# Performance work log

Measured on AMD Instinct MI355X. Metric: run time of the kernel, lower is better.

The kernel has to match this reference:

```python
import jax, jax.numpy as jnp
import numpy as np


def _bag_mean(idx, table):
    # F.embedding_bag(mode='mean', padding_idx=last row): padding entries are
    # excluded from both the sum and the count. idx: [B, S, K]
    pad = table.shape[0] - 1
    mask = (idx != pad)[..., None].astype(table.dtype)          # [B,S,K,1]
    emb = table[idx] * mask                                      # [B,S,K,D]
    cnt = mask.sum(axis=-2)                                      # [B,S,1]
    s = emb.sum(axis=-2)                                         # [B,S,D]
    return jnp.where(cnt > 0, s / jnp.maximum(cnt, 1.0), 0.0)


def _subgraph_parts(qq, ques_table, skill_table, diff_table, area_table,
                    ques2skill, ques2diff, ques2area):
    qe = ques_table[qq]                                          # [B,S,D]
    sk = _bag_mean(ques2skill[qq], skill_table)                  # [B,S,D]
    df = diff_table[ques2diff[qq][..., 0]]                       # [B,S,D]
    ar = area_table[ques2area[qq][..., 0]]                       # [B,S,D]
    return qe, sk, df, ar


def reference(q, a, next_q, ques_table, skill_table, diff_table, area_table,
              ques2skill, ques2diff, ques2area, Wq, bq):
    # ---- get_subgraph_embedding (non-JunYi path) ----
    qe, sk, df, ar = _subgraph_parts(q, ques_table, skill_table, diff_table,
                                     area_table, ques2skill, ques2diff, ques2area)
    q_emb = (qe + sk + df + ar) / 4.0

    nqe, nsk, ndf, nar = _subgraph_parts(next_q, ques_table, skill_table,
                                         diff_table, area_table, ques2skill,
                                         ques2diff, ques2area)
    nq_emb = (nqe + nsk + ndf + nar) / 4.0
    # faithful to source: the averaging line for next_q is applied twice
    nq_emb = (nq_emb + nsk + ndf + nar) / 4.0

    q_emb = q_emb @ Wq.T + bq
    nq_emb = nq_emb @ Wq.T + bq

    # ---- Fusion_Module: answer==1 keeps first half, answer==0 keeps second ----
    af = a[..., None].astype(q_emb.dtype)                        # [B,S,1]
    input_emb = jnp.concatenate([q_emb * af, q_emb * (1.0 - af)], axis=-1)

    return jnp.concatenate([input_emb, nq_emb], axis=-1)        # [B,S,3D]


def setup_inputs() -> dict:
    key = jax.random.key(0)
    ks = jax.random.split(key, 12)
    B, S, D = 16, 2048, 128
    NQ, NS, ND, NA, K = 200001, 2001, 100, 50, 8
    return {
        "q": jax.random.randint(ks[0], (B, S), 0, NQ - 1),
        "a": jax.random.randint(ks[1], (B, S), 0, 2),
        "next_q": jax.random.randint(ks[2], (B, S), 0, NQ - 1),
        "ques_table": jax.random.normal(ks[3], (NQ, D), jnp.float32),
        "skill_table": jax.random.normal(ks[4], (NS, D), jnp.float32),
        "diff_table": jax.random.normal(ks[5], (ND, D), jnp.float32),
        "area_table": jax.random.normal(ks[6], (NA, D), jnp.float32),
        "ques2skill": jax.random.randint(ks[7], (NQ, K), 0, NS),
        "ques2diff": jax.random.randint(ks[8], (NQ, 1), 0, ND),
        "ques2area": jax.random.randint(ks[9], (NQ, 1), 0, NA),
        "Wq": jax.random.normal(ks[10], (D, D), jnp.float32) / np.sqrt(D),
        "bq": jax.random.normal(ks[11], (D,), jnp.float32) * 0.01,
    }
```

## Files before the change

### kernel.cpp

```cpp
#include <hip/hip_runtime.h>
#include <hip/hip_bf16.h>

typedef float  f32x4  __attribute__((ext_vector_type(4)));
typedef short  s16x8  __attribute__((ext_vector_type(8)));

#define PIN_LOADS() asm volatile("" ::: "memory")

__device__ __forceinline__ unsigned short f2bf(float f) {
    unsigned int u = __float_as_uint(f);
    unsigned int rnd = 0x7fffu + ((u >> 16) & 1u);
    return (unsigned short)((u + rnd) >> 16);
}

__device__ __forceinline__ void bf8_fma(const s16x8 v, float s, f32x4& a0, f32x4& a1) {
    const uint4 u = *(const uint4*)&v;
    a0[0] += s * __uint_as_float(u.x << 16);
    a0[1] += s * __uint_as_float(u.x & 0xffff0000u);
    a0[2] += s * __uint_as_float(u.y << 16);
    a0[3] += s * __uint_as_float(u.y & 0xffff0000u);
    a1[0] += s * __uint_as_float(u.z << 16);
    a1[1] += s * __uint_as_float(u.z & 0xffff0000u);
    a1[2] += s * __uint_as_float(u.w << 16);
    a1[3] += s * __uint_as_float(u.w & 0xffff0000u);
}

__global__ __launch_bounds__(256)
void h2kt_prep(const float* __restrict__ Wq,
               const float* __restrict__ skill, const float* __restrict__ diff,
               const float* __restrict__ area,
               const int* __restrict__ q, const int* __restrict__ next_q,
               const int* __restrict__ a_arr,
               const int* __restrict__ q2s, const int* __restrict__ q2d,
               const int* __restrict__ q2a,
               unsigned short* __restrict__ Wqb,
               unsigned short* __restrict__ T2,
               int* __restrict__ desc,
               int pad_idx)
{
    const int bid = blockIdx.x, tid = threadIdx.x;

    if (bid < 8) {
        const int s  = bid * 256 + tid;
        const int f  = s >> 6, sl = s & 63;
        const int jt = f >> 2, kt = f & 3;
        const int row = jt * 16 + (sl & 15);
        const int col = kt * 32 + (sl >> 4) * 8;
        const float4 w0 = *(const float4*)(Wq + row * 128 + col);
        const float4 w1 = *(const float4*)(Wq + row * 128 + col + 4);
        s16x8 v;
        v[0] = (short)f2bf(w0.x); v[1] = (short)f2bf(w0.y);
        v[2] = (short)f2bf(w0.z); v[3] = (short)f2bf(w0.w);
        v[4] = (short)f2bf(w1.x); v[5] = (short)f2bf(w1.y);
        v[6] = (short)f2bf(w1.z); v[7] = (short)f2bf(w1.w);
        *(s16x8*)(Wqb + (size_t)s * 8) = v;
    } else if (bid < 42) {
        const int lane = tid & 63;
        const int cl = lane & 15, grp = lane >> 4;
        const int row16 = ((bid - 8) * 4 + (tid >> 6)) * 16;
        if (row16 > 2150) return;

        int srow = row16 + cl;
        if (srow > 2150) srow = 2150;
        const float* src = (srow < 2001) ? skill + (size_t)srow * 128
                         : (srow < 2101) ? diff + (size_t)(srow - 2001) * 128
                                         : area + (size_t)(srow - 2101) * 128;
        s16x8 afr[4];
        #pragma unroll
        for (int kt = 0; kt < 4; ++kt) {
            const float4 v0 = *(const float4*)(src + kt * 32 + grp * 8);
            const float4 v1 = *(const float4*)(src + kt * 32 + grp * 8 + 4);
            s16x8 v;
            v[0] = (short)f2bf(v0.x); v[1] = (short)f2bf(v0.y);
            v[2] = (short)f2bf(v0.z); v[3] = (short)f2bf(v0.w);
            v[4] = (short)f2bf(v1.x); v[5] = (short)f2bf(v1.y);
            v[6] = (short)f2bf(v1.z); v[7] = (short)f2bf(v1.w);
            afr[kt] = v;
        }
        #pragma unroll
        for (int jt = 0; jt < 8; ++jt) {
            f32x4 acc = {0.f, 0.f, 0.f, 0.f};
            #pragma unroll
            for (int kt = 0; kt < 4; ++kt) {
                const float* wp = Wq + (jt * 16 + cl) * 128 + kt * 32 + grp * 8;
                const float4 w0 = *(const float4*)(wp);
                const float4 w1 = *(const float4*)(wp + 4);
                s16x8 bf;
                bf[0] = (short)f2bf(w0.x); bf[1] = (short)f2bf(w0.y);
                bf[2] = (short)f2bf(w0.z); bf[3] = (short)f2bf(w0.w);
                bf[4] = (short)f2bf(w1.x); bf[5] = (short)f2bf(w1.y);
                bf[6] = (short)f2bf(w1.z); bf[7] = (short)f2bf(w1.w);
                acc = __builtin_amdgcn_mfma_f32_16x16x32_bf16(afr[kt], bf, acc, 0, 0, 0);
            }
            #pragma unroll
            for (int r = 0; r < 4; ++r) {
                const int orow = row16 + grp * 4 + r;
                if (orow < 2151) T2[(size_t)orow * 128 + jt * 16 + cl] = f2bf(acc[r]);
            }
        }
    } else {
        const int g = (bid - 42) * 256 + tid;
        const int p = g & 32767;
        const bool isnq = (g >= 32768);
        const int qq = isnq ? next_q[p] : q[p];
        const int4 s03 = *(const int4*)(q2s + (size_t)qq * 8);
        const int4 s47 = *(const int4*)(q2s + (size_t)qq * 8 + 4);
        const int di = q2d[qq];
        const int ai = q2a[qq];
        const int av = isnq ? 1 : a_arr[p];
        int4* d = (int4*)(desc + (size_t)g * 12);
        d[0] = make_int4(qq, s03.x, s03.y, s03.z);
        d[1] = make_int4(s03.w, s47.x, s47.y, s47.z);
        d[2] = make_int4(s47.w, 2001 + di, 2101 + ai, av);
    }
}

__global__ __launch_bounds__(128, 4)
void h2kt_fused(const int* __restrict__ desc,
                const float* __restrict__ ques_table,
                const unsigned short* __restrict__ T2,
                const unsigned short* __restrict__ Wqb,
                const float* __restrict__ bq,
                float* __restrict__ out,
                int pad_idx)
{
    __shared__ __align__(16) unsigned char U[16 * 132 * 4];
    unsigned short* Q = (unsigned short*)U;
    float*          D = (float*)U;

    const int tid  = threadIdx.x;
    const int w    = tid >> 6;
    const int lane = tid & 63;
    const int cl   = lane & 15;
    const int grp  = lane >> 4;
    const int g0   = blockIdx.x * 16;
    const int base = g0 & 32767;
    const bool isnq = (g0 >= 32768);
    const float wq_ = isnq ? 0.0625f : 0.25f;
    const float wr_ = isnq ? 0.3125f : 0.25f;

    const int r2 = lane >> 5;
    const int c  = lane & 31;
    int qqv[4];
    #pragma unroll
    for (int p = 0; p < 4; ++p)
        qqv[p] = desc[(size_t)(g0 + w * 8 + p * 2 + r2) * 12];

    const int4* D0 = (const int4*)(desc + (size_t)(g0 + w * 8 + grp) * 12);
    const int4* D1 = (const int4*)(desc + (size_t)(g0 + w * 8 + 4 + grp) * 12);
    const int4 a0i = D0[0], a1i = D0[1], a2i = D0[2];
    const int4 b0i = D1[0], b1i = D1[1], b2i = D1[2];

    f32x4 qv[4];
    #pragma unroll
    for (int p = 0; p < 4; ++p)
        qv[p] = *(const f32x4*)(ques_table + (size_t)qqv[p] * 128 + c * 4);

    const int sa[8] = {a0i.y, a0i.z, a0i.w, a1i.x, a1i.y, a1i.z, a1i.w, a2i.x};
    const int sb[8] = {b0i.y, b0i.z, b0i.w, b1i.x, b1i.y, b1i.z, b1i.w, b2i.x};
    const int av0 = a2i.w, av1 = b2i.w;

    s16x8 t0[10];
    #pragma unroll
    for (int i = 0; i < 8; ++i)
        t0[i] = *(const s16x8*)(T2 + (size_t)sa[i] * 128 + cl * 8);
    t0[8] = *(const s16x8*)(T2 + (size_t)a2i.y * 128 + cl * 8);
    t0[9] = *(const s16x8*)(T2 + (size_t)a2i.z * 128 + cl * 8);
    PIN_LOADS();

    #pragma unroll
    for (int p = 0; p < 4; ++p) {
        ushort4 o;
        o.x = f2bf(wq_ * qv[p][0]); o.y = f2bf(wq_ * qv[p][1]);
        o.z = f2bf(wq_ * qv[p][2]); o.w = f2bf(wq_ * qv[p][3]);
        *(ushort4*)(Q + (size_t)(w * 8 + p * 2 + r2) * 136 + c * 4) = o;
    }

    s16x8 t1[10];
    #pragma unroll
    for (int i = 0; i < 8; ++i)
        t1[i] = *(const s16x8*)(T2 + (size_t)sb[i] * 128 + cl * 8);
    t1[8] = *(const s16x8*)(T2 + (size_t)b2i.y * 128 + cl * 8);
    t1[9] = *(const s16x8*)(T2 + (size_t)b2i.z * 128 + cl * 8);
    PIN_LOADS();

    int cnt0 = 0, cnt1 = 0;
    #pragma unroll
    for (int i = 0; i < 8; ++i) { cnt0 += (sa[i] != pad_idx); cnt1 += (sb[i] != pad_idx); }
    const float cs0 = cnt0 > 0 ? wr_ / (float)cnt0 : 0.f;
    const float cs1 = cnt1 > 0 ? wr_ / (float)cnt1 : 0.f;

    f32x4 restA[2], restB[2];
    {
        f32x4 a0 = {0.f,0.f,0.f,0.f}, a1 = {0.f,0.f,0.f,0.f};
        #pragma unroll
        for (int i = 0; i < 8; ++i) bf8_fma(t0[i], (sa[i] != pad_idx) ? cs0 : 0.f, a0, a1);
        bf8_fma(t0[8], wr_, a0, a1);
        bf8_fma(t0[9], wr_, a0, a1);
        restA[0] = a0; restB[0] = a1;
    }
    {
        f32x4 a0 = {0.f,0.f,0.f,0.f}, a1 = {0.f,0.f,0.f,0.f};
        #pragma unroll
        for (int i = 0; i < 8; ++i) bf8_fma(t1[i], (sb[i] != pad_idx) ? cs1 : 0.f, a0, a1);
        bf8_fma(t1[8], wr_, a0, a1);
        bf8_fma(t1[9], wr_, a0, a1);
        restA[1] = a0; restB[1] = a1;
    }

    __syncthreads();

    s16x8 afr[4];
    #pragma unroll
    for (int kt = 0; kt < 4; ++kt)
        afr[kt] = *(const s16x8*)(Q + (size_t)cl * 136 + kt * 32 + grp * 8);

    __syncthreads();

    #pragma unroll
    for (int jt2 = 0; jt2 < 4; ++jt2) {
        const int jt = w * 4 + jt2;
        f32x4 acc = {0.f, 0.f, 0.f, 0.f};
        #pragma unroll
        for (int kt = 0; kt < 4; ++kt) {
            const s16x8 bf = *(const s16x8*)(Wqb + ((size_t)(jt * 4 + kt) * 64 + lane) * 8);
            acc = __builtin_amdgcn_mfma_f32_16x16x32_bf16(afr[kt], bf, acc, 0, 0, 0);
        }
        #pragma unroll
        for (int r = 0; r < 4; ++r)
            D[(size_t)(grp * 4 + r) * 132 + jt * 16 + cl] = acc[r];
    }

    __syncthreads();

    const f32x4 bq0 = *(const f32x4*)(bq + cl * 8);
    const f32x4 bq1 = *(const f32x4*)(bq + cl * 8 + 4);
    const f32x4 z = {0.f, 0.f, 0.f, 0.f};
    #pragma unroll
    for (int p = 0; p < 2; ++p) {
        const int row = w * 8 + p * 4 + grp;
        const f32x4 d0 = *(const f32x4*)(D + (size_t)row * 132 + cl * 8);
        const f32x4 d1 = *(const f32x4*)(D + (size_t)row * 132 + cl * 8 + 4);
        const f32x4 v0 = d0 + restA[p] + bq0;
        const f32x4 v1 = d1 + restB[p] + bq1;
        const size_t orow = (size_t)(base + row);
        const int avv = (p == 0) ? av0 : av1;
        if (!isnq) {
            const bool on = (avv != 0);
            *(f32x4*)(out + orow * 384 + cl * 8)           = on ? v0 : z;
            *(f32x4*)(out + orow * 384 + cl * 8 + 4)       = on ? v1 : z;
            *(f32x4*)(out + orow * 384 + 128 + cl * 8)     = on ? z : v0;
            *(f32x4*)(out + orow * 384 + 128 + cl * 8 + 4) = on ? z : v1;
        } else {
            *(f32x4*)(out + orow * 384 + 256 + cl * 8)     = v0;
            *(f32x4*)(out + orow * 384 + 256 + cl * 8 + 4) = v1;
        }
    }
}

extern "C" void kernel_launch(void* const* d_in, const int* in_sizes, int n_in,
                              void* d_out, int out_size, void* d_ws, size_t ws_size,
                              hipStream_t stream) {
    const int*   q          = (const int*)d_in[0];
    const int*   a          = (const int*)d_in[1];
    const int*   next_q     = (const int*)d_in[2];
    const float* ques_table = (const float*)d_in[3];
    const float* skill_tab  = (const float*)d_in[4];
    const float* diff_tab   = (const float*)d_in[5];
    const float* area_tab   = (const float*)d_in[6];
    const int*   q2s        = (const int*)d_in[7];
    const int*   q2d        = (const int*)d_in[8];
    const int*   q2a        = (const int*)d_in[9];
    const float* Wq         = (const float*)d_in[10];
    const float* bq         = (const float*)d_in[11];
    float* out = (float*)d_out;

    const int NS = in_sizes[4] / 128;
    const int pad_idx = NS - 1;

    int*            descp = (int*)d_ws;
    unsigned short* Wqb   = (unsigned short*)((char*)d_ws + (size_t)65536 * 48);
    unsigned short* T2    = Wqb + (size_t)2048 * 8;

    h2kt_prep<<<298, 256, 0, stream>>>(Wq, skill_tab, diff_tab, area_tab,
                                       q, next_q, a, q2s, q2d, q2a,
                                       Wqb, T2, descp, pad_idx);
    h2kt_fused<<<4096, 128, 0, stream>>>(descp, ques_table, T2, Wqb, bq, out, pad_idx);
}
```

Before: 42.91 us.

## Process two tiles per block and prefetch next tile's descriptors and question rows

Each block now handles two 16-row tiles in sequence. While the first tile computes, it prefetches the second tile's descriptors and ques_table rows. Q and D get separate shared buffers, which removes one barrier, and the second bag's loads are reordered to overlap with the first bag's FMAs. The grid is halved and launch bounds are lowered to 3 waves per SIMD. This trades occupancy and extra registers for software-pipelined latency hiding on the gather-bound path.

Result: slower. 65.68 us (+53.1%).

```diff
diff --git a/kernel.cpp b/kernel.cpp
--- a/kernel.cpp
+++ b/kernel.cpp
@@ -114,74 +114,69 @@
     }
 }
 
-__global__ __launch_bounds__(128, 4)
-void h2kt_fused(const int* __restrict__ desc,
-                const float* __restrict__ ques_table,
-                const unsigned short* __restrict__ T2,
-                const unsigned short* __restrict__ Wqb,
-                const float* __restrict__ bq,
-                float* __restrict__ out,
-                int pad_idx)
+struct TI { int q0, q1, q2, q3; int4 a0, a1, a2, b0, b1, b2; };
+
+__device__ __forceinline__ void load_desc(const int* __restrict__ desc, int g0,
+                                          int w, int r2, int grp, TI& ti) {
+    ti.q0 = desc[(size_t)(g0 + w * 8 + 0 + r2) * 12];
+    ti.q1 = desc[(size_t)(g0 + w * 8 + 2 + r2) * 12];
+    ti.q2 = desc[(size_t)(g0 + w * 8 + 4 + r2) * 12];
+    ti.q3 = desc[(size_t)(g0 + w * 8 + 6 + r2) * 12];
+    const int4* P0 = (const int4*)(desc + (size_t)(g0 + w * 8 + grp) * 12);
+    const int4* P1 = (const int4*)(desc + (size_t)(g0 + w * 8 + 4 + grp) * 12);
+    ti.a0 = P0[0]; ti.a1 = P0[1]; ti.a2 = P0[2];
+    ti.b0 = P1[0]; ti.b1 = P1[1]; ti.b2 = P1[2];
+}
+
+__device__ __forceinline__ void issue_qe(const float* __restrict__ ques, const TI& ti,
+                                         int c, f32x4& v0, f32x4& v1, f32x4& v2, f32x4& v3) {
+    v0 = *(const f32x4*)(ques + (size_t)ti.q0 * 128 + c * 4);
+    v1 = *(const f32x4*)(ques + (size_t)ti.q1 * 128 + c * 4);
+    v2 = *(const f32x4*)(ques + (size_t)ti.q2 * 128 + c * 4);
+    v3 = *(const f32x4*)(ques + (size_t)ti.q3 * 128 + c * 4);
+}
+
+template<int PRE>
+__device__ __forceinline__ void do_tile(
+    const int* __restrict__ desc, const float* __restrict__ ques,
+    const unsigned short* __restrict__ T2, const unsigned short* __restrict__ Wqb,
+    const float* __restrict__ bq, float* __restrict__ out,
+    unsigned short* Q, float* D,
+    int obase, bool isnq, float wq_, float wr_, int pad_idx,
+    int w, int lane, int cl, int grp, int r2, int c,
+    const TI& cur, f32x4 qv0, f32x4 qv1, f32x4 qv2, f32x4 qv3,
+    int next_g0, TI& nxt, f32x4& nq0, f32x4& nq1, f32x4& nq2, f32x4& nq3)
 {
-    __shared__ __align__(16) unsigned char U[16 * 132 * 4];
-    unsigned short* Q = (unsigned short*)U;
-    float*          D = (float*)U;
-
-    const int tid  = threadIdx.x;
-    const int w    = tid >> 6;
-    const int lane = tid & 63;
-    const int cl   = lane & 15;
-    const int grp  = lane >> 4;
-    const int g0   = blockIdx.x * 16;
-    const int base = g0 & 32767;
-    const bool isnq = (g0 >= 32768);
-    const float wq_ = isnq ? 0.0625f : 0.25f;
-    const float wr_ = isnq ? 0.3125f : 0.25f;
-
-    const int r2 = lane >> 5;
-    const int c  = lane & 31;
-    int qqv[4];
-    #pragma unroll
-    for (int p = 0; p < 4; ++p)
-        qqv[p] = desc[(size_t)(g0 + w * 8 + p * 2 + r2) * 12];
-
-    const int4* D0 = (const int4*)(desc + (size_t)(g0 + w * 8 + grp) * 12);
-    const int4* D1 = (const int4*)(desc + (size_t)(g0 + w * 8 + 4 + grp) * 12);
-    const int4 a0i = D0[0], a1i = D0[1], a2i = D0[2];
-    const int4 b0i = D1[0], b1i = D1[1], b2i = D1[2];
-
-    f32x4 qv[4];
-    #pragma unroll
-    for (int p = 0; p < 4; ++p)
-        qv[p] = *(const f32x4*)(ques_table + (size_t)qqv[p] * 128 + c * 4);
-
-    const int sa[8] = {a0i.y, a0i.z, a0i.w, a1i.x, a1i.y, a1i.z, a1i.w, a2i.x};
-    const int sb[8] = {b0i.y, b0i.z, b0i.w, b1i.x, b1i.y, b1i.z, b1i.w, b2i.x};
-    const int av0 = a2i.w, av1 = b2i.w;
+    const int sa[8] = {cur.a0.y, cur.a0.z, cur.a0.w, cur.a1.x,
+                       cur.a1.y, cur.a1.z, cur.a1.w, cur.a2.x};
+    const int sb[8] = {cur.b0.y, cur.b0.z, cur.b0.w, cur.b1.x,
+                       cur.b1.y, cur.b1.z, cur.b1.w, cur.b2.x};
 
     s16x8 t0[10];
     #pragma unroll
     for (int i = 0; i < 8; ++i)
         t0[i] = *(const s16x8*)(T2 + (size_t)sa[i] * 128 + cl * 8);
-    t0[8] = *(const s16x8*)(T2 + (size_t)a2i.y * 128 + cl * 8);
-    t0[9] = *(const s16x8*)(T2 + (size_t)a2i.z * 128 + cl * 8);
+    t0[8] = *(const s16x8*)(T2 + (size_t)cur.a2.y * 128 + cl * 8);
+    t0[9] = *(const s16x8*)(T2 + (size_t)cur.a2.z * 128 + cl * 8);
     PIN_LOADS();
 
-    #pragma unroll
-    for (int p = 0; p < 4; ++p) {
+    if (PRE) load_desc(desc, next_g0, w, r2, grp, nxt);
+
+    {
         ushort4 o;
-        o.x = f2bf(wq_ * qv[p][0]); o.y = f2bf(wq_ * qv[p][1]);
-        o.z = f2bf(wq_ * qv[p][2]); o.w = f2bf(wq_ * qv[p][3]);
-        *(ushort4*)(Q + (size_t)(w * 8 + p * 2 + r2) * 136 + c * 4) = o;
-    }
-
-    s16x8 t1[10];
-    #pragma unroll
-    for (int i = 0; i < 8; ++i)
-        t1[i] = *(const s16x8*)(T2 + (size_t)sb[i] * 128 + cl * 8);
-    t1[8] = *(const s16x8*)(T2 + (size_t)b2i.y * 128 + cl * 8);
-    t1[9] = *(const s16x8*)(T2 + (size_t)b2i.z * 128 + cl * 8);
-    PIN_LOADS();
+        o.x = f2bf(wq_ * qv0[0]); o.y = f2bf(wq_ * qv0[1]);
+        o.z = f2bf(wq_ * qv0[2]); o.w = f2bf(wq_ * qv0[3]);
+        *(ushort4*)(Q + (size_t)(w * 8 + 0 + r2) * 136 + c * 4) = o;
+        o.x = f2bf(wq_ * qv1[0]); o.y = f2bf(wq_ * qv1[1]);
+        o.z = f2bf(wq_ * qv1[2]); o.w = f2bf(wq_ * qv1[3]);
+        *(ushort4*)(Q + (size_t)(w * 8 + 2 + r2) * 136 + c * 4) = o;
+        o.x = f2bf(wq_ * qv2[0]); o.y = f2bf(wq_ * qv2[1]);
+        o.z = f2bf(wq_ * qv2[2]); o.w = f2bf(wq_ * qv2[3]);
+        *(ushort4*)(Q + (size_t)(w * 8 + 4 + r2) * 136 + c * 4) = o;
+        o.x = f2bf(wq_ * qv3[0]); o.y = f2bf(wq_ * qv3[1]);
+        o.z = f2bf(wq_ * qv3[2]); o.w = f2bf(wq_ * qv3[3]);
+        *(ushort4*)(Q + (size_t)(w * 8 + 6 + r2) * 136 + c * 4) = o;
+    }
 
     int cnt0 = 0, cnt1 = 0;
     #pragma unroll
@@ -189,23 +184,30 @@
     const float cs0 = cnt0 > 0 ? wr_ / (float)cnt0 : 0.f;
     const float cs1 = cnt1 > 0 ? wr_ / (float)cnt1 : 0.f;
 
-    f32x4 restA[2], restB[2];
-    {
-        f32x4 a0 = {0.f,0.f,0.f,0.f}, a1 = {0.f,0.f,0.f,0.f};
-        #pragma unroll
-        for (int i = 0; i < 8; ++i) bf8_fma(t0[i], (sa[i] != pad_idx) ? cs0 : 0.f, a0, a1);
-        bf8_fma(t0[8], wr_, a0, a1);
-        bf8_fma(t0[9], wr_, a0, a1);
-        restA[0] = a0; restB[0] = a1;
-    }
-    {
-        f32x4 a0 = {0.f,0.f,0.f,0.f}, a1 = {0.f,0.f,0.f,0.f};
-        #pragma unroll
-        for (int i = 0; i < 8; ++i) bf8_fma(t1[i], (sb[i] != pad_idx) ? cs1 : 0.f, a0, a1);
-        bf8_fma(t1[8], wr_, a0, a1);
-        bf8_fma(t1[9], wr_, a0, a1);
-        restA[1] = a0; restB[1] = a1;
-    }
+    f32x4 rA0 = {0,0,0,0}, rB0 = {0,0,0,0};
+    #pragma unroll
+    for (int i = 0; i < 8; ++i) bf8_fma(t0[i], (sa[i] != pad_idx) ? cs0 : 0.f, rA0, rB0);
+    bf8_fma(t0[8], wr_, rA0, rB0);
+    bf8_fma(t0[9], wr_, rA0, rB0);
+
+    s16x8 t1[10];
+    #pragma unroll
+    for (int i = 0; i < 8; ++i)
+        t1[i] = *(const s16x8*)(T2 + (size_t)sb[i] * 128 + cl * 8);
+    t1[8] = *(const s16x8*)(T2 + (size_t)cur.b2.y * 128 + cl * 8);
+    t1[9] = *(const s16x8*)(T2 + (size_t)cur.b2.z * 128 + cl * 8);
+    PIN_LOADS();
+
+    if (PRE) {
+        issue_qe(ques, nxt, c, nq0, nq1, nq2, nq3);
+        PIN_LOADS();
+    }
+
+    f32x4 rA1 = {0,0,0,0}, rB1 = {0,0,0,0};
+    #pragma unroll
+    for (int i = 0; i < 8; ++i) bf8_fma(t1[i], (sb[i] != pad_idx) ? cs1 : 0.f, rA1, rB1);
+    bf8_fma(t1[8], wr_, rA1, rB1);
+    bf8_fma(t1[9], wr_, rA1, rB1);
 
     __syncthreads();
 
@@ -213,8 +215,6 @@
     #pragma unroll
     for (int kt = 0; kt < 4; ++kt)
         afr[kt] = *(const s16x8*)(Q + (size_t)cl * 136 + kt * 32 + grp * 8);
-
-    __syncthreads();
 
     #pragma unroll
     for (int jt2 = 0; jt2 < 4; ++jt2) {
@@ -240,10 +240,10 @@
         const int row = w * 8 + p * 4 + grp;
         const f32x4 d0 = *(const f32x4*)(D + (size_t)row * 132 + cl * 8);
         const f32x4 d1 = *(const f32x4*)(D + (size_t)row * 132 + cl * 8 + 4);
-        const f32x4 v0 = d0 + restA[p] + bq0;
-        const f32x4 v1 = d1 + restB[p] + bq1;
-        const size_t orow = (size_t)(base + row);
-        const int avv = (p == 0) ? av0 : av1;
+        const f32x4 v0 = d0 + (p == 0 ? rA0 : rA1) + bq0;
+        const f32x4 v1 = d1 + (p == 0 ? rB0 : rB1) + bq1;
+        const size_t orow = (size_t)(obase + row);
+        const int avv = (p == 0) ? cur.a2.w : cur.b2.w;
         if (!isnq) {
             const bool on = (avv != 0);
             *(f32x4*)(out + orow * 384 + cl * 8)           = on ? v0 : z;
@@ -255,6 +255,55 @@
             *(f32x4*)(out + orow * 384 + 256 + cl * 8 + 4) = v1;
         }
     }
+
+    __syncthreads();
+}
+
+__global__ __launch_bounds__(128, 3)
+void h2kt_fused(const int* __restrict__ desc,
+                const float* __restrict__ ques_table,
+                const unsigned short* __restrict__ T2,
+                const unsigned short* __restrict__ Wqb,
+                const float* __restrict__ bq,
+                float* __restrict__ out,
+                int pad_idx)
+{
+    __shared__ __align__(16) unsigned short Q[16 * 136];
+    __shared__ __align__(16) float          D[16 * 132];
+
+    const int tid  = threadIdx.x;
+    const int w    = tid >> 6;
+    const int lane = tid & 63;
+    const int cl   = lane & 15;
+    const int grp  = lane >> 4;
+    const int r2   = lane >> 5;
+    const int c    = lane & 31;
+
+    const int bid = blockIdx.x;
+    const int gA  = bid * 32;
+    const int gB  = gA + 16;
+    const bool isnq = (gA >= 32768);
+    const float wq_ = isnq ? 0.0625f : 0.25f;
+    const float wr_ = isnq ? 0.3125f : 0.25f;
+
+    TI tiA, tiB;
+    f32x4 qa0, qa1, qa2, qa3, qb0, qb1, qb2, qb3;
+
+    load_desc(desc, gA, w, r2, grp, tiA);
+    issue_qe(ques_table, tiA, c, qa0, qa1, qa2, qa3);
+    PIN_LOADS();
+
+    do_tile<1>(desc, ques_table, T2, Wqb, bq, out, Q, D,
+               gA & 32767, isnq, wq_, wr_, pad_idx,
+               w, lane, cl, grp, r2, c,
+               tiA, qa0, qa1, qa2, qa3,
+               gB, tiB, qb0, qb1, qb2, qb3);
+
+    do_tile<0>(desc, ques_table, T2, Wqb, bq, out, Q, D,
+               gB & 32767, isnq, wq_, wr_, pad_idx,
+               w, lane, cl, grp, r2, c,
+               tiB, qb0, qb1, qb2, qb3,
+               gB, tiA, qa0, qa1, qa2, qa3);
 }
 
 extern "C" void kernel_launch(void* const* d_in, const int* in_sizes, int n_in,
@@ -284,5 +333,5 @@
     h2kt_prep<<<298, 256, 0, stream>>>(Wq, skill_tab, diff_tab, area_tab,
                                        q, next_q, a, q2s, q2d, q2a,
                                        Wqb, T2, descp, pad_idx);
-    h2kt_fused<<<4096, 128, 0, stream>>>(descp, ques_table, T2, Wqb, bq, out, pad_idx);
-}
+    h2kt_fused<<<2048, 128, 0, stream>>>(descp, ques_table, T2, Wqb, bq, out, pad_idx);
+}
```

## Split fused kernel into separate question-projection and gather-combine kernels

Applied to the files above, without the earlier changes.

Splits the single fused kernel into two. A 64-thread kernel gathers ques_table rows, projects them through Wq with MFMA and writes the result as bf16 to a workspace buffer. A second 256-thread kernel gathers the skill/diff/area rows, adds the stored projection and bias, and writes the output. The aim is to remove the shared-memory staging and barriers that coupled the gathers to the matmul, and to give each stage its own occupancy. The cost is an extra launch and a workspace write plus read of the intermediate, and the projection is now rounded to bf16 where it used to stay in fp32.

Result: slower. 45.04 us (+5.0%).

```diff
diff --git a/kernel.cpp b/kernel.cpp
--- a/kernel.cpp
+++ b/kernel.cpp
@@ -3,8 +3,6 @@
 
 typedef float  f32x4  __attribute__((ext_vector_type(4)));
 typedef short  s16x8  __attribute__((ext_vector_type(8)));
-
-#define PIN_LOADS() asm volatile("" ::: "memory")
 
 __device__ __forceinline__ unsigned short f2bf(float f) {
     unsigned int u = __float_as_uint(f);
@@ -114,146 +112,126 @@
     }
 }
 
-__global__ __launch_bounds__(128, 4)
-void h2kt_fused(const int* __restrict__ desc,
-                const float* __restrict__ ques_table,
+__global__ __launch_bounds__(64)
+void h2kt_e0(const int* __restrict__ q, const int* __restrict__ next_q,
+             const float* __restrict__ ques_table,
+             const unsigned short* __restrict__ Wqb,
+             unsigned short* __restrict__ D0)
+{
+    __shared__ __align__(16) float D[16 * 132];
+
+    const int lane = threadIdx.x;
+    const int cl = lane & 15, grp = lane >> 4;
+    const int g0 = blockIdx.x * 16;
+    const int base = g0 & 32767;
+    const bool isnq = (g0 >= 32768);
+    const float wq_ = isnq ? 0.0625f : 0.25f;
+
+    const int qq = (isnq ? next_q : q)[base + cl];
+    const float* qrow = ques_table + (size_t)qq * 128 + grp * 8;
+
+    s16x8 afr[4];
+    #pragma unroll
+    for (int kt = 0; kt < 4; ++kt) {
+        const f32x4 a = *(const f32x4*)(qrow + kt * 32);
+        const f32x4 b = *(const f32x4*)(qrow + kt * 32 + 4);
+        s16x8 v;
+        #pragma unroll
+        for (int j = 0; j < 4; ++j) {
+            v[j]     = (short)f2bf(wq_ * a[j]);
+            v[j + 4] = (short)f2bf(wq_ * b[j]);
+        }
+        afr[kt] = v;
+    }
+
+    #pragma unroll
+    for (int jt = 0; jt < 8; ++jt) {
+        f32x4 acc = {0.f, 0.f, 0.f, 0.f};
+        #pragma unroll
+        for (int kt = 0; kt < 4; ++kt) {
+            const s16x8 bf = *(const s16x8*)(Wqb + ((size_t)(jt * 4 + kt) * 64 + lane) * 8);
+            acc = __builtin_amdgcn_mfma_f32_16x16x32_bf16(afr[kt], bf, acc, 0, 0, 0);
+        }
+        #pragma unroll
+        for (int r = 0; r < 4; ++r)
+            D[(size_t)(grp * 4 + r) * 132 + jt * 16 + cl] = acc[r];
+    }
+
+    __syncthreads();
+
+    #pragma unroll
+    for (int p = 0; p < 4; ++p) {
+        const int row = p * 4 + grp;
+        const f32x4 d0 = *(const f32x4*)(D + (size_t)row * 132 + cl * 8);
+        const f32x4 d1 = *(const f32x4*)(D + (size_t)row * 132 + cl * 8 + 4);
+        s16x8 v;
+        #pragma unroll
+        for (int j = 0; j < 4; ++j) {
+            v[j]     = (short)f2bf(d0[j]);
+            v[j + 4] = (short)f2bf(d1[j]);
+        }
+        *(s16x8*)(D0 + (size_t)(g0 + row) * 128 + cl * 8) = v;
+    }
+}
+
+__global__ __launch_bounds__(256, 2)
+void h2kt_final(const int* __restrict__ desc,
+                const unsigned short* __restrict__ D0,
                 const unsigned short* __restrict__ T2,
-                const unsigned short* __restrict__ Wqb,
                 const float* __restrict__ bq,
                 float* __restrict__ out,
                 int pad_idx)
 {
-    __shared__ __align__(16) unsigned char U[16 * 132 * 4];
-    unsigned short* Q = (unsigned short*)U;
-    float*          D = (float*)U;
-
     const int tid  = threadIdx.x;
     const int w    = tid >> 6;
     const int lane = tid & 63;
     const int cl   = lane & 15;
     const int grp  = lane >> 4;
-    const int g0   = blockIdx.x * 16;
-    const int base = g0 & 32767;
-    const bool isnq = (g0 >= 32768);
-    const float wq_ = isnq ? 0.0625f : 0.25f;
+    const int g    = blockIdx.x * 16 + w * 4 + grp;
+    const int orow = g & 32767;
+    const bool isnq = (g >= 32768);
     const float wr_ = isnq ? 0.3125f : 0.25f;
 
-    const int r2 = lane >> 5;
-    const int c  = lane & 31;
-    int qqv[4];
-    #pragma unroll
-    for (int p = 0; p < 4; ++p)
-        qqv[p] = desc[(size_t)(g0 + w * 8 + p * 2 + r2) * 12];
-
-    const int4* D0 = (const int4*)(desc + (size_t)(g0 + w * 8 + grp) * 12);
-    const int4* D1 = (const int4*)(desc + (size_t)(g0 + w * 8 + 4 + grp) * 12);
-    const int4 a0i = D0[0], a1i = D0[1], a2i = D0[2];
-    const int4 b0i = D1[0], b1i = D1[1], b2i = D1[2];
-
-    f32x4 qv[4];
-    #pragma unroll
-    for (int p = 0; p < 4; ++p)
-        qv[p] = *(const f32x4*)(ques_table + (size_t)qqv[p] * 128 + c * 4);
-
-    const int sa[8] = {a0i.y, a0i.z, a0i.w, a1i.x, a1i.y, a1i.z, a1i.w, a2i.x};
-    const int sb[8] = {b0i.y, b0i.z, b0i.w, b1i.x, b1i.y, b1i.z, b1i.w, b2i.x};
-    const int av0 = a2i.w, av1 = b2i.w;
-
-    s16x8 t0[10];
+    const int4* P = (const int4*)(desc + (size_t)g * 12);
+    const int4 i0 = P[0], i1 = P[1], i2 = P[2];
+    const int sa[8] = {i0.y, i0.z, i0.w, i1.x, i1.y, i1.z, i1.w, i2.x};
+
+    const s16x8 dv = *(const s16x8*)(D0 + (size_t)g * 128 + cl * 8);
+
+    s16x8 t[10];
     #pragma unroll
     for (int i = 0; i < 8; ++i)
-        t0[i] = *(const s16x8*)(T2 + (size_t)sa[i] * 128 + cl * 8);
-    t0[8] = *(const s16x8*)(T2 + (size_t)a2i.y * 128 + cl * 8);
-    t0[9] = *(const s16x8*)(T2 + (size_t)a2i.z * 128 + cl * 8);
-    PIN_LOADS();
-
-    #pragma unroll
-    for (int p = 0; p < 4; ++p) {
-        ushort4 o;
-        o.x = f2bf(wq_ * qv[p][0]); o.y = f2bf(wq_ * qv[p][1]);
-        o.z = f2bf(wq_ * qv[p][2]); o.w = f2bf(wq_ * qv[p][3]);
-        *(ushort4*)(Q + (size_t)(w * 8 + p * 2 + r2) * 136 + c * 4) = o;
-    }
-
-    s16x8 t1[10];
-    #pragma unroll
-    for (int i = 0; i < 8; ++i)
-        t1[i] = *(const s16x8*)(T2 + (size_t)sb[i] * 128 + cl * 8);
-    t1[8] = *(const s16x8*)(T2 + (size_t)b2i.y * 128 + cl * 8);
-    t1[9] = *(const s16x8*)(T2 + (size_t)b2i.z * 128 + cl * 8);
-    PIN_LOADS();
-
-    int cnt0 = 0, cnt1 = 0;
-    #pragma unroll
-    for (int i = 0; i < 8; ++i) { cnt0 += (sa[i] != pad_idx); cnt1 += (sb[i] != pad_idx); }
-    const float cs0 = cnt0 > 0 ? wr_ / (float)cnt0 : 0.f;
-    const float cs1 = cnt1 > 0 ? wr_ / (float)cnt1 : 0.f;
-
-    f32x4 restA[2], restB[2];
-    {
-        f32x4 a0 = {0.f,0.f,0.f,0.f}, a1 = {0.f,0.f,0.f,0.f};
-        #pragma unroll
-        for (int i = 0; i < 8; ++i) bf8_fma(t0[i], (sa[i] != pad_idx) ? cs0 : 0.f, a0, a1);
-        bf8_fma(t0[8], wr_, a0, a1);
-        bf8_fma(t0[9], wr_, a0, a1);
-        restA[0] = a0; restB[0] = a1;
-    }
-    {
-        f32x4 a0 = {0.f,0.f,0.f,0.f}, a1 = {0.f,0.f,0.f,0.f};
-        #pragma unroll
-        for (int i = 0; i < 8; ++i) bf8_fma(t1[i], (sb[i] != pad_idx) ? cs1 : 0.f, a0, a1);
-        bf8_fma(t1[8], wr_, a0, a1);
-        bf8_fma(t1[9], wr_, a0, a1);
-        restA[1] = a0; restB[1] = a1;
-    }
-
-    __syncthreads();
-
-    s16x8 afr[4];
-    #pragma unroll
-    for (int kt = 0; kt < 4; ++kt)
-        afr[kt] = *(const s16x8*)(Q + (size_t)cl * 136 + kt * 32 + grp * 8);
-
-    __syncthreads();
-
-    #pragma unroll
-    for (int jt2 = 0; jt2 < 4; ++jt2) {
-        const int jt = w * 4 + jt2;
-        f32x4 acc = {0.f, 0.f, 0.f, 0.f};
-        #pragma unroll
-        for (int kt = 0; kt < 4; ++kt) {
-            const s16x8 bf = *(const s16x8*)(Wqb + ((size_t)(jt * 4 + kt) * 64 + lane) * 8);
-            acc = __builtin_amdgcn_mfma_f32_16x16x32_bf16(afr[kt], bf, acc, 0, 0, 0);
-        }
-        #pragma unroll
-        for (int r = 0; r < 4; ++r)
-            D[(size_t)(grp * 4 + r) * 132 + jt * 16 + cl] = acc[r];
-    }
-
-    __syncthreads();
+        t[i] = *(const s16x8*)(T2 + (size_t)sa[i] * 128 + cl * 8);
+    t[8] = *(const s16x8*)(T2 + (size_t)i2.y * 128 + cl * 8);
+    t[9] = *(const s16x8*)(T2 + (size_t)i2.z * 128 + cl * 8);
+
+    int cnt = 0;
+    #pragma unroll
+    for (int i = 0; i < 8; ++i) cnt += (sa[i] != pad_idx);
+    const float cs = cnt > 0 ? wr_ / (float)cnt : 0.f;
+
+    f32x4 a0 = {0,0,0,0}, a1 = {0,0,0,0};
+    #pragma unroll
+    for (int i = 0; i < 8; ++i) bf8_fma(t[i], (sa[i] != pad_idx) ? cs : 0.f, a0, a1);
+    bf8_fma(t[8], wr_, a0, a1);
+    bf8_fma(t[9], wr_, a0, a1);
+    bf8_fma(dv, 1.f, a0, a1);
 
     const f32x4 bq0 = *(const f32x4*)(bq + cl * 8);
     const f32x4 bq1 = *(const f32x4*)(bq + cl * 8 + 4);
+    const f32x4 v0 = a0 + bq0;
+    const f32x4 v1 = a1 + bq1;
     const f32x4 z = {0.f, 0.f, 0.f, 0.f};
-    #pragma unroll
-    for (int p = 0; p < 2; ++p) {
-        const int row = w * 8 + p * 4 + grp;
-        const f32x4 d0 = *(const f32x4*)(D + (size_t)row * 132 + cl * 8);
-        const f32x4 d1 = *(const f32x4*)(D + (size_t)row * 132 + cl * 8 + 4);
-        const f32x4 v0 = d0 + restA[p] + bq0;
-        const f32x4 v1 = d1 + restB[p] + bq1;
-        const size_t orow = (size_t)(base + row);
-        const int avv = (p == 0) ? av0 : av1;
-        if (!isnq) {
-            const bool on = (avv != 0);
-            *(f32x4*)(out + orow * 384 + cl * 8)           = on ? v0 : z;
-            *(f32x4*)(out + orow * 384 + cl * 8 + 4)       = on ? v1 : z;
-            *(f32x4*)(out + orow * 384 + 128 + cl * 8)     = on ? z : v0;
-            *(f32x4*)(out + orow * 384 + 128 + cl * 8 + 4) = on ? z : v1;
-        } else {
-            *(f32x4*)(out + orow * 384 + 256 + cl * 8)     = v0;
-            *(f32x4*)(out + orow * 384 + 256 + cl * 8 + 4) = v1;
-        }
+
+    if (!isnq) {
+        const bool on = (i2.w != 0);
+        *(f32x4*)(out + (size_t)orow * 384 + cl * 8)           = on ? v0 : z;
+        *(f32x4*)(out + (size_t)orow * 384 + cl * 8 + 4)       = on ? v1 : z;
+        *(f32x4*)(out + (size_t)orow * 384 + 128 + cl * 8)     = on ? z : v0;
+        *(f32x4*)(out + (size_t)orow * 384 + 128 + cl * 8 + 4) = on ? z : v1;
+    } else {
+        *(f32x4*)(out + (size_t)orow * 384 + 256 + cl * 8)     = v0;
+        *(f32x4*)(out + (size_t)orow * 384 + 256 + cl * 8 + 4) = v1;
     }
 }
 
@@ -277,12 +255,14 @@
     const int NS = in_sizes[4] / 128;
     const int pad_idx = NS - 1;
 
-    int*            descp = (int*)d_ws;
-    unsigned short* Wqb   = (unsigned short*)((char*)d_ws + (size_t)65536 * 48);
+    unsigned short* D0    = (unsigned short*)d_ws;
+    int*            descp = (int*)((char*)d_ws + (size_t)65536 * 256);
+    unsigned short* Wqb   = (unsigned short*)((char*)descp + (size_t)65536 * 48);
     unsigned short* T2    = Wqb + (size_t)2048 * 8;
 
     h2kt_prep<<<298, 256, 0, stream>>>(Wq, skill_tab, diff_tab, area_tab,
                                        q, next_q, a, q2s, q2d, q2a,
                                        Wqb, T2, descp, pad_idx);
-    h2kt_fused<<<4096, 128, 0, stream>>>(descp, ques_table, T2, Wqb, bq, out, pad_idx);
-}
+    h2kt_e0<<<4096, 64, 0, stream>>>(q, next_q, ques_table, Wqb, D0);
+    h2kt_final<<<4096, 256, 0, stream>>>(descp, D0, T2, bq, out, pad_idx);
+}
```
